# Kernel tuning notes

Measured on AMD Instinct MI355X. Metric: run time of the kernel, lower is better.

The kernel has to match this reference:

```python
import jax, jax.numpy as jnp
import numpy as np
from jax import lax

B, N, D = 4, 4096, 1024
H, DH, K = 8, 128, 256  # heads, dim_head, linformer k
KERNEL = 32
PAD = (15, 16)  # torch padding='same' for even kernel: left=(k-1)//2, right=rest


def setup_inputs() -> dict:
    key = jax.random.key(0)
    ks = jax.random.split(key, 7)
    s = 0.02
    return {
        "x": jax.random.normal(ks[0], (B, N, D), dtype=jnp.float32),
        "Wq": jax.random.normal(ks[1], (D, D), dtype=jnp.float32) * s,
        "Wk": jax.random.normal(ks[2], (D, D), dtype=jnp.float32) * s,
        "Wpk": jax.random.normal(ks[3], (K, N, KERNEL), dtype=jnp.float32) * s,
        "bpk": jax.random.normal(ks[4], (K,), dtype=jnp.float32) * s,
        "Wo": jax.random.normal(ks[5], (D, D), dtype=jnp.float32) * s,
        "bo": jax.random.normal(ks[6], (D,), dtype=jnp.float32) * s,
    }


def reference(x, Wq, Wk, Wpk, bpk, Wo, bo):
    b, n, d = x.shape
    # linear projections (torch Linear: y = x @ W.T)
    q = x @ Wq.T                       # (b, n, h*dh)
    keys = x @ Wk.T                    # (b, n, h*dh)
    # Conv1d over feature length with seq positions as channels: (b, n, d) -> (b, k, d)
    keys = lax.conv_general_dilated(
        keys, Wpk, window_strides=(1,), padding=[PAD],
        dimension_numbers=("NCH", "OIH", "NCH"),
    ) + bpk[None, :, None]             # (b, K, h*dh)
    values = keys                      # share_kv=True
    # split heads
    q = q.reshape(b, n, H, DH).transpose(0, 2, 1, 3)        # (b, h, n, dh)
    kk = keys.reshape(b, K, H, DH).transpose(0, 2, 1, 3)    # (b, h, K, dh)
    vv = values.reshape(b, K, H, DH).transpose(0, 2, 1, 3)  # (b, h, K, dh)
    dots = jnp.einsum("bhnd,bhkd->bhnk", q, kk) * (DH ** -0.5)
    attn = jax.nn.softmax(dots, axis=-1)                    # dropout p=0.0 (eval)
    out = jnp.einsum("bhnk,bhkd->bhnd", attn, vv)
    out = out.transpose(0, 2, 1, 3).reshape(b, n, H * DH)
    return out @ Wo.T + bo
```

## Files before the change

kernel.cpp:

```cpp
#include <hip/hip_runtime.h>


typedef short v8s __attribute__((ext_vector_type(8)));
typedef float v4f __attribute__((ext_vector_type(4)));

#define MFMA16(a, b, c) __builtin_amdgcn_mfma_f32_16x16x32_bf16((a), (b), (c), 0, 0, 0)

__device__ __forceinline__ unsigned short f2bf(float f) {
  unsigned int u = __float_as_uint(f);
  u += 0x7fffu + ((u >> 16) & 1u);
  return (unsigned short)(u >> 16);
}

__device__ __forceinline__ v8s cvt8(float4 a, float4 b) {
  v8s v;
  v[0] = (short)f2bf(a.x); v[1] = (short)f2bf(a.y);
  v[2] = (short)f2bf(a.z); v[3] = (short)f2bf(a.w);
  v[4] = (short)f2bf(b.x); v[5] = (short)f2bf(b.y);
  v[6] = (short)f2bf(b.z); v[7] = (short)f2bf(b.w);
  return v;
}

__global__ __launch_bounds__(256) void k_reorder_wpk(const float* __restrict__ Wpk,
                                                     short* __restrict__ Wr) {
  __shared__ short T[64][40];
  const int k  = blockIdx.x >> 6;
  const int n0 = (blockIdx.x & 63) << 6;
  const int tid = threadIdx.x;
  {
    const int i = tid >> 2, t0 = (tid & 3) << 3;
    const float* p = Wpk + ((size_t)k * 4096 + n0 + i) * 32 + t0;
    float4 a = *(const float4*)p, b = *(const float4*)(p + 4);
    *(v8s*)&T[i][t0] = cvt8(a, b);
  }
  __syncthreads();
  {
    const int t = tid >> 3, j0 = (tid & 7) << 3;
    v8s o;
#pragma unroll
    for (int q = 0; q < 8; ++q) o[q] = T[j0 + q][t];
    *(v8s*)(Wr + ((size_t)t * 256 + k) * 4096 + n0 + j0) = o;
  }
}

__global__ __launch_bounds__(256) void k_init_kc(const float* __restrict__ bpk,
                                                 float* __restrict__ Kc) {
  const int idx = (blockIdx.x * 256 + threadIdx.x) * 4;
  const float v = bpk[(idx >> 10) & 255];
  float4 f; f.x = v; f.y = v; f.z = v; f.w = v;
  *(float4*)(Kc + idx) = f;
}

__global__ __launch_bounds__(256) void k_gemm_qk(const float* __restrict__ x,
                                                 const float* __restrict__ Wq,
                                                 const float* __restrict__ Wk,
                                                 short* __restrict__ Qbf,
                                                 short* __restrict__ Kp) {
  __shared__ short As[128][40];
  __shared__ short Bs[128][40];
  const int tid = threadIdx.x;
  const int m0 = blockIdx.x * 128;
  const int j0 = blockIdx.y * 128;
  const int lane = tid & 63, w = tid >> 6;
  const int wr = (w >> 1) * 64, wc = (w & 1) * 64;
  const int l15 = lane & 15, lg8 = (lane >> 4) * 8;

  v4f acc[4][4];
#pragma unroll
  for (int i = 0; i < 4; ++i)
#pragma unroll
    for (int j = 0; j < 4; ++j) acc[i][j] = (v4f)0.0f;

  for (int k0 = 0; k0 < 1024; k0 += 32) {
#pragma unroll
    for (int c = 0; c < 2; ++c) {
      const int cid = tid + (c << 8);
      const int r = cid >> 2, sg = (cid & 3) << 3;
      const float* pa = x + (size_t)(m0 + r) * 1024 + k0 + sg;
      *(v8s*)&As[r][sg] = cvt8(*(const float4*)pa, *(const float4*)(pa + 4));
      const int J = j0 + r;
      const float* pb = (J < 1024 ? Wq + (size_t)J * 1024
                                  : Wk + (size_t)(J - 1024) * 1024) + k0 + sg;
      *(v8s*)&Bs[r][sg] = cvt8(*(const float4*)pb, *(const float4*)(pb + 4));
    }
    __syncthreads();
    v8s af[4], bfr[4];
#pragma unroll
    for (int mi = 0; mi < 4; ++mi) af[mi] = *(const v8s*)&As[wr + mi * 16 + l15][lg8];
#pragma unroll
    for (int ni = 0; ni < 4; ++ni) bfr[ni] = *(const v8s*)&Bs[wc + ni * 16 + l15][lg8];
#pragma unroll
    for (int ni = 0; ni < 4; ++ni)
#pragma unroll
      for (int mi = 0; mi < 4; ++mi)
        acc[mi][ni] = MFMA16(af[mi], bfr[ni], acc[mi][ni]);
    __syncthreads();
  }
  const int rbase = (lane >> 4) * 4;
#pragma unroll
  for (int mi = 0; mi < 4; ++mi)
#pragma unroll
    for (int ni = 0; ni < 4; ++ni) {
      const int col = j0 + wc + ni * 16 + l15;
      short* dst = (col < 1024) ? Qbf : Kp;
      const int cj = (col < 1024) ? col : col - 1024;
#pragma unroll
      for (int r = 0; r < 4; ++r) {
        const int row = m0 + wr + mi * 16 + rbase + r;
        dst[(size_t)row * 1024 + cj] = (short)f2bf(acc[mi][ni][r]);
      }
    }
}

__global__ __launch_bounds__(256) void k_transpose(const short* __restrict__ src,
                                                   short* __restrict__ dst,
                                                   int R, int C) {
  __shared__ short T[64][72];
  const int r0 = blockIdx.x * 64, c0 = blockIdx.y * 64;
  const size_t sb = (size_t)blockIdx.z * R * C;
  const int tid = threadIdx.x;
  {
    const int i = tid >> 2, q = (tid & 3) << 4;
    const short* ps = src + sb + (size_t)(r0 + i) * C + c0 + q;
    *(v8s*)&T[i][q]     = *(const v8s*)ps;
    *(v8s*)&T[i][q + 8] = *(const v8s*)(ps + 8);
  }
  __syncthreads();
  {
    const int j = tid >> 2, p = (tid & 3) << 4;
    v8s o0, o1;
#pragma unroll
    for (int t = 0; t < 8; ++t) o0[t] = T[p + t][j];
#pragma unroll
    for (int t = 0; t < 8; ++t) o1[t] = T[p + 8 + t][j];
    short* pd = dst + sb + (size_t)(c0 + j) * R + r0 + p;
    *(v8s*)pd = o0;
    *(v8s*)(pd + 8) = o1;
  }
}

__global__ __launch_bounds__(256) void k_conv(const short* __restrict__ Wr,
                                              const short* __restrict__ KpT,
                                              float* __restrict__ Kc) {
  __shared__ short Kt[159][40];
  __shared__ short As[4][128][40];
  const int bx = blockIdx.x;
  const int b = bx & 3, ns = (bx >> 2) & 7, nt = (bx >> 5) & 7, mt = bx >> 8;
  const int K0 = mt * 128, D0 = nt * 128;
  const int tid = threadIdx.x;
  const int lane = tid & 63, w = tid >> 6;
  const int wr = (w >> 1) * 64, wc = (w & 1) * 64;
  const int l15 = lane & 15, lg8 = (lane >> 4) * 8;
  const size_t kpt_b = (size_t)b * 1024 * 4096;

  v4f acc[4][4];
#pragma unroll
  for (int i = 0; i < 4; ++i)
#pragma unroll
    for (int j = 0; j < 4; ++j) acc[i][j] = (v4f)0.0f;

#pragma unroll 1
  for (int nc = 0; nc < 16; ++nc) {
    const int n0 = ns * 512 + nc * 32;
    __syncthreads();
#pragma unroll
    for (int it = 0; it < 3; ++it) {
      const int s = it * 256 + tid;
      if (s < 636) {
        const int r = s >> 2, sg = (s & 3) << 3;
        const int dp = D0 - 15 + r;
        v8s v = {0, 0, 0, 0, 0, 0, 0, 0};
        if (dp >= 0 && dp < 1024)
          v = *(const v8s*)(KpT + kpt_b + (size_t)dp * 4096 + n0 + sg);
        *(v8s*)&Kt[r][sg] = v;
      }
    }
#pragma unroll 1
    for (int tc = 0; tc < 8; ++tc) {
      const int t0 = tc * 4;
      __syncthreads();
#pragma unroll
      for (int i = 0; i < 8; ++i) {
        const int s = i * 256 + tid;
        const int tt = s >> 9, rr = (s >> 2) & 127, sg = (s & 3) << 3;
        *(v8s*)&As[tt][rr][sg] =
            *(const v8s*)(Wr + ((size_t)(t0 + tt) * 256 + K0 + rr) * 4096 + n0 + sg);
      }
      __syncthreads();
#pragma unroll
      for (int tt = 0; tt < 4; ++tt) {
        const int s = t0 + tt;
        v8s af[4], bfr[4];
#pragma unroll
        for (int mi = 0; mi < 4; ++mi)
          af[mi] = *(const v8s*)&As[tt][wr + mi * 16 + l15][lg8];
#pragma unroll
        for (int ni = 0; ni < 4; ++ni)
          bfr[ni] = *(const v8s*)&Kt[wc + ni * 16 + l15 + s][lg8];
#pragma unroll
        for (int ni = 0; ni < 4; ++ni)
#pragma unroll
          for (int mi = 0; mi < 4; ++mi)
            acc[mi][ni] = MFMA16(af[mi], bfr[ni], acc[mi][ni]);
      }
    }
  }
  float* kcb = Kc + (size_t)b * 256 * 1024;
  const int rbase = (lane >> 4) * 4;
#pragma unroll
  for (int mi = 0; mi < 4; ++mi)
#pragma unroll
    for (int ni = 0; ni < 4; ++ni)
#pragma unroll
      for (int r = 0; r < 4; ++r)
        atomicAdd(kcb + (size_t)(K0 + wr + mi * 16 + rbase + r) * 1024 +
                      (D0 + wc + ni * 16 + l15),
                  acc[mi][ni][r]);
}

__global__ __launch_bounds__(256) void k_kc_post(const float* __restrict__ Kc,
                                                 short* __restrict__ Kcbf,
                                                 short* __restrict__ KcT) {
  __shared__ short T[64][72];
  const int k0 = blockIdx.x * 64, d0 = blockIdx.y * 64, b = blockIdx.z;
  const int tid = threadIdx.x;
  {
    const int i = tid >> 2, q = (tid & 3) << 4;
    const float* ps = Kc + (size_t)(b * 256 + k0 + i) * 1024 + d0 + q;
    float4 f0 = *(const float4*)ps,       f1 = *(const float4*)(ps + 4);
    float4 f2 = *(const float4*)(ps + 8), f3 = *(const float4*)(ps + 12);
    v8s v0 = cvt8(f0, f1), v1 = cvt8(f2, f3);
    *(v8s*)&T[i][q] = v0;
    *(v8s*)&T[i][q + 8] = v1;
    short* pc = Kcbf + (size_t)(b * 256 + k0 + i) * 1024 + d0 + q;
    *(v8s*)pc = v0;
    *(v8s*)(pc + 8) = v1;
  }
  __syncthreads();
  {
    const int j = tid >> 2, p = (tid & 3) << 4;
    v8s o0, o1;
#pragma unroll
    for (int t = 0; t < 8; ++t) o0[t] = T[p + t][j];
#pragma unroll
    for (int t = 0; t < 8; ++t) o1[t] = T[p + 8 + t][j];
    short* pd = KcT + (size_t)(b * 1024 + d0 + j) * 256 + k0 + p;
    *(v8s*)pd = o0;
    *(v8s*)(pd + 8) = o1;
  }
}

__global__ __launch_bounds__(256) void k_attn(const short* __restrict__ Qbf,
                                              const short* __restrict__ Kcbf,
                                              const short* __restrict__ KcT,
                                              short* __restrict__ AO) {
  __shared__ short P[4][16][264];
  const int nt = blockIdx.x, h = blockIdx.y, b = blockIdx.z;
  const int tid = threadIdx.x, lane = tid & 63, w = tid >> 6;
  const int l15 = lane & 15, lg4 = (lane >> 4) * 4, lg8 = (lane >> 4) * 8;
  const float scale = 0.08838834764831845f;
  const size_t qb  = (size_t)b * 4096 * 1024 + (size_t)h * 128;
  const size_t kb  = (size_t)b * 256 * 1024 + (size_t)h * 128;
  const size_t vtb = ((size_t)b * 1024 + (size_t)h * 128) * 256;
  short (*Pw)[264] = P[w];
  const int n_wave = nt * 128 + w * 32;

#pragma unroll 1
  for (int half = 0; half < 2; ++half) {
    const int nbase = n_wave + half * 16;
    v8s aq[4];
#pragma unroll
    for (int kt = 0; kt < 4; ++kt)
      aq[kt] = *(const v8s*)(Qbf + qb + (size_t)(nbase + l15) * 1024 + kt * 32 + lg8);

    v4f dacc[16];
#pragma unroll
    for (int ct = 0; ct < 16; ++ct) dacc[ct] = (v4f)0.0f;
#pragma unroll 1
    for (int kt = 0; kt < 4; ++kt) {
#pragma unroll
      for (int ct = 0; ct < 16; ++ct) {
        v8s bk = *(const v8s*)(Kcbf + kb + (size_t)(ct * 16 + l15) * 1024 + kt * 32 + lg8);
        dacc[ct] = MFMA16(aq[kt], bk, dacc[ct]);
      }
    }
#pragma unroll
    for (int ct = 0; ct < 16; ++ct) dacc[ct] = dacc[ct] * scale;
    v4f m4 = dacc[0];
#pragma unroll
    for (int ct = 1; ct < 16; ++ct)
#pragma unroll
      for (int r = 0; r < 4; ++r) m4[r] = fmaxf(m4[r], dacc[ct][r]);
#pragma unroll
    for (int off = 1; off < 16; off <<= 1)
#pragma unroll
      for (int r = 0; r < 4; ++r) m4[r] = fmaxf(m4[r], __shfl_xor(m4[r], off, 64));
    v4f ssum = (v4f)0.0f;
#pragma unroll
    for (int ct = 0; ct < 16; ++ct)
#pragma unroll
      for (int r = 0; r < 4; ++r) {
        const float e = __expf(dacc[ct][r] - m4[r]);
        ssum[r] += e;
        Pw[lg4 + r][ct * 16 + l15] = (short)f2bf(e);
      }
#pragma unroll
    for (int off = 1; off < 16; off <<= 1)
#pragma unroll
      for (int r = 0; r < 4; ++r) ssum[r] += __shfl_xor(ssum[r], off, 64);
    __syncthreads();

    v4f oacc[8];
#pragma unroll
    for (int ct = 0; ct < 8; ++ct) oacc[ct] = (v4f)0.0f;
#pragma unroll 1
    for (int kt2 = 0; kt2 < 8; ++kt2) {
      v8s pa = *(const v8s*)&Pw[l15][kt2 * 32 + lg8];
#pragma unroll
      for (int ct = 0; ct < 8; ++ct) {
        v8s bv = *(const v8s*)(KcT + vtb + (size_t)(ct * 16 + l15) * 256 + kt2 * 32 + lg8);
        oacc[ct] = MFMA16(pa, bv, oacc[ct]);
      }
    }
    v4f inv;
#pragma unroll
    for (int r = 0; r < 4; ++r) inv[r] = 1.0f / ssum[r];
#pragma unroll
    for (int ct = 0; ct < 8; ++ct)
#pragma unroll
      for (int r = 0; r < 4; ++r)
        AO[qb + (size_t)(nbase + lg4 + r) * 1024 + ct * 16 + l15] =
            (short)f2bf(oacc[ct][r] * inv[r]);
    __syncthreads();
  }
}

__global__ __launch_bounds__(256) void k_gemm_out(const short* __restrict__ AO,
                                                  const float* __restrict__ Wo,
                                                  const float* __restrict__ bo,
                                                  float* __restrict__ out) {
  __shared__ short As[128][40];
  __shared__ short Bs[128][40];
  const int tid = threadIdx.x;
  const int m0 = blockIdx.x * 128;
  const int j0 = blockIdx.y * 128;
  const int lane = tid & 63, w = tid >> 6;
  const int wr = (w >> 1) * 64, wc = (w & 1) * 64;
  const int l15 = lane & 15, lg8 = (lane >> 4) * 8;

  v4f acc[4][4];
#pragma unroll
  for (int i = 0; i < 4; ++i)
#pragma unroll
    for (int j = 0; j < 4; ++j) acc[i][j] = (v4f)0.0f;

  for (int k0 = 0; k0 < 1024; k0 += 32) {
#pragma unroll
    for (int c = 0; c < 2; ++c) {
      const int cid = tid + (c << 8);
      const int r = cid >> 2, sg = (cid & 3) << 3;
      *(v8s*)&As[r][sg] = *(const v8s*)(AO + (size_t)(m0 + r) * 1024 + k0 + sg);
      const float* pb = Wo + (size_t)(j0 + r) * 1024 + k0 + sg;
      *(v8s*)&Bs[r][sg] = cvt8(*(const float4*)pb, *(const float4*)(pb + 4));
    }
    __syncthreads();
    v8s af[4], bfr[4];
#pragma unroll
    for (int mi = 0; mi < 4; ++mi) af[mi] = *(const v8s*)&As[wr + mi * 16 + l15][lg8];
#pragma unroll
    for (int ni = 0; ni < 4; ++ni) bfr[ni] = *(const v8s*)&Bs[wc + ni * 16 + l15][lg8];
#pragma unroll
    for (int ni = 0; ni < 4; ++ni)
#pragma unroll
      for (int mi = 0; mi < 4; ++mi)
        acc[mi][ni] = MFMA16(af[mi], bfr[ni], acc[mi][ni]);
    __syncthreads();
  }
  const int rbase = (lane >> 4) * 4;
#pragma unroll
  for (int mi = 0; mi < 4; ++mi)
#pragma unroll
    for (int ni = 0; ni < 4; ++ni) {
      const int col = j0 + wc + ni * 16 + l15;
      const float bias = bo[col];
#pragma unroll
      for (int r = 0; r < 4; ++r) {
        const int row = m0 + wr + mi * 16 + rbase + r;
        out[(size_t)row * 1024 + col] = acc[mi][ni][r] + bias;
      }
    }
}

extern "C" void kernel_launch(void* const* d_in, const int* in_sizes, int n_in,
                              void* d_out, int out_size, void* d_ws, size_t ws_size,
                              hipStream_t stream) {
  const float* x   = (const float*)d_in[0];
  const float* Wq  = (const float*)d_in[1];
  const float* Wk  = (const float*)d_in[2];
  const float* Wpk = (const float*)d_in[3];
  const float* bpk = (const float*)d_in[4];
  const float* Wo  = (const float*)d_in[5];
  const float* bo  = (const float*)d_in[6];

  const size_t OFF_WR   = 0;
  const size_t OFF_QBF  = 67108864;
  const size_t OFF_KP   = 100663296;
  const size_t OFF_KPT  = 134217728;
  const size_t OFF_KC   = 167772160;
  const size_t OFF_KCBF = 171966464;
  const size_t OFF_KCT  = 174063616;
  const size_t NEED     = 176160768;
  if (ws_size < NEED) return;

  char* ws = (char*)d_ws;
  short* Wr   = (short*)(ws + OFF_WR);
  short* Qbf  = (short*)(ws + OFF_QBF);
  short* Kp   = (short*)(ws + OFF_KP);
  short* KpT  = (short*)(ws + OFF_KPT);
  float* Kc   = (float*)(ws + OFF_KC);
  short* Kcbf = (short*)(ws + OFF_KCBF);
  short* KcT  = (short*)(ws + OFF_KCT);
  short* AO   = Kp;
  float* outp = (float*)d_out;

  k_reorder_wpk<<<dim3(16384), dim3(256), 0, stream>>>(Wpk, Wr);
  k_init_kc<<<dim3(1024), dim3(256), 0, stream>>>(bpk, Kc);
  k_gemm_qk<<<dim3(128, 16), dim3(256), 0, stream>>>(x, Wq, Wk, Qbf, Kp);
  k_transpose<<<dim3(64, 16, 4), dim3(256), 0, stream>>>(Kp, KpT, 4096, 1024);
  k_conv<<<dim3(512), dim3(256), 0, stream>>>(Wr, KpT, Kc);
  k_kc_post<<<dim3(4, 16, 4), dim3(256), 0, stream>>>(Kc, Kcbf, KcT);
  k_attn<<<dim3(32, 8, 4), dim3(256), 0, stream>>>(Qbf, Kcbf, KcT, AO);
  k_gemm_out<<<dim3(128, 8), dim3(256), 0, stream>>>(AO, Wo, bo, outp);
}
```

Baseline: 741.0 us.

## Double-buffer GEMMs and conv with direct global-to-LDS loads and swizzled layout

Converts x, Wq/Wk and Wo to bf16 in separate passes so the GEMMs can stream bf16 tiles with global_load_lds into double-buffered, XOR-swizzled LDS. This overlaps loads with MFMA work and avoids bank conflicts. The conv kernel gets the same treatment, plus a zero-padded transposed K buffer that removes boundary checks and an XCD-aware block remapping. It adds extra conversion and padding launches and reuses workspace regions, which carries an aliasing risk.

```diff
diff --git a/kernel.cpp b/kernel.cpp
--- a/kernel.cpp
+++ b/kernel.cpp
@@ -21,6 +21,24 @@
   return v;
 }
 
+__device__ __forceinline__ void gld16(void* lds, const void* g) {
+  __builtin_amdgcn_global_load_lds(
+      (const __attribute__((address_space(1))) void*)g,
+      (__attribute__((address_space(3))) void*)lds, 16, 0, 0);
+}
+
+__device__ __forceinline__ const v8s* frag_ptr(const short* base, int row, int g) {
+  return (const v8s*)(base + row * 32 + (((g ^ (row >> 1)) & 3) << 3));
+}
+
+__global__ __launch_bounds__(256) void k_cvt(const float* __restrict__ src,
+                                             short* __restrict__ dst, int n8) {
+  const int i = blockIdx.x * 256 + threadIdx.x;
+  if (i >= n8) return;
+  const float4* s = (const float4*)src;
+  ((v8s*)dst)[i] = cvt8(s[2 * i], s[2 * i + 1]);
+}
+
 __global__ __launch_bounds__(256) void k_reorder_wpk(const float* __restrict__ Wpk,
                                                      short* __restrict__ Wr) {
   __shared__ short T[64][40];
@@ -51,19 +69,26 @@
   *(float4*)(Kc + idx) = f;
 }
 
-__global__ __launch_bounds__(256) void k_gemm_qk(const float* __restrict__ x,
-                                                 const float* __restrict__ Wq,
-                                                 const float* __restrict__ Wk,
-                                                 short* __restrict__ Qbf,
-                                                 short* __restrict__ Kp) {
-  __shared__ short As[128][40];
-  __shared__ short Bs[128][40];
-  const int tid = threadIdx.x;
-  const int m0 = blockIdx.x * 128;
-  const int j0 = blockIdx.y * 128;
-  const int lane = tid & 63, w = tid >> 6;
+__global__ __launch_bounds__(256) void k_zero_pad(short* __restrict__ KpTp) {
+  const int idx = blockIdx.x * 256 + threadIdx.x;
+  const int ridx = idx >> 9, col8 = idx & 511;
+  const int b = ridx >> 5, rr = ridx & 31;
+  const int row = (rr < 15) ? rr : 1039 + (rr - 15);
+  v8s z = {0, 0, 0, 0, 0, 0, 0, 0};
+  *(v8s*)(KpTp + ((size_t)b * 1056 + row) * 4096 + col8 * 8) = z;
+}
+
+__global__ __launch_bounds__(256) void k_gemm_qk_v2(const short* __restrict__ xbf,
+                                                    const short* __restrict__ Wqk,
+                                                    short* __restrict__ Qbf,
+                                                    short* __restrict__ Kp) {
+  __shared__ short As[2][128][32];
+  __shared__ short Bs[2][128][32];
+  const int tid = threadIdx.x, lane = tid & 63, w = tid >> 6;
+  const int m0 = blockIdx.x * 128, j0 = blockIdx.y * 128;
   const int wr = (w >> 1) * 64, wc = (w & 1) * 64;
-  const int l15 = lane & 15, lg8 = (lane >> 4) * 8;
+  const int l15 = lane & 15, g = lane >> 4;
+  const int sr = lane >> 2, sseg = lane & 3;
 
   v4f acc[4][4];
 #pragma unroll
@@ -71,29 +96,33 @@
 #pragma unroll
     for (int j = 0; j < 4; ++j) acc[i][j] = (v4f)0.0f;
 
-  for (int k0 = 0; k0 < 1024; k0 += 32) {
-#pragma unroll
-    for (int c = 0; c < 2; ++c) {
-      const int cid = tid + (c << 8);
-      const int r = cid >> 2, sg = (cid & 3) << 3;
-      const float* pa = x + (size_t)(m0 + r) * 1024 + k0 + sg;
-      *(v8s*)&As[r][sg] = cvt8(*(const float4*)pa, *(const float4*)(pa + 4));
-      const int J = j0 + r;
-      const float* pb = (J < 1024 ? Wq + (size_t)J * 1024
-                                  : Wk + (size_t)(J - 1024) * 1024) + k0 + sg;
-      *(v8s*)&Bs[r][sg] = cvt8(*(const float4*)pb, *(const float4*)(pb + 4));
-    }
-    __syncthreads();
-    v8s af[4], bfr[4];
-#pragma unroll
-    for (int mi = 0; mi < 4; ++mi) af[mi] = *(const v8s*)&As[wr + mi * 16 + l15][lg8];
-#pragma unroll
-    for (int ni = 0; ni < 4; ++ni) bfr[ni] = *(const v8s*)&Bs[wc + ni * 16 + l15][lg8];
+  auto stage = [&](int buf, int k0) {
+#pragma unroll
+    for (int q0 = 0; q0 < 2; ++q0) {
+      const int rblk = (w * 2 + q0) << 4, r = rblk + sr;
+      const int co = ((sseg ^ (r >> 1)) & 3) << 3;
+      gld16(&As[buf][rblk][0], xbf + (size_t)(m0 + r) * 1024 + k0 + co);
+      gld16(&Bs[buf][rblk][0], Wqk + (size_t)(j0 + r) * 1024 + k0 + co);
+    }
+  };
+
+  stage(0, 0);
+  __syncthreads();
+#pragma unroll 1
+  for (int k0 = 0, buf = 0; k0 < 1024; k0 += 32, buf ^= 1) {
+    if (k0 + 32 < 1024) stage(buf ^ 1, k0 + 32);
+    v8s af[4], bf4[4];
+#pragma unroll
+    for (int mi = 0; mi < 4; ++mi)
+      af[mi] = *frag_ptr(&As[buf][0][0], wr + mi * 16 + l15, g);
 #pragma unroll
     for (int ni = 0; ni < 4; ++ni)
+      bf4[ni] = *frag_ptr(&Bs[buf][0][0], wc + ni * 16 + l15, g);
+#pragma unroll
+    for (int ni = 0; ni < 4; ++ni)
 #pragma unroll
       for (int mi = 0; mi < 4; ++mi)
-        acc[mi][ni] = MFMA16(af[mi], bfr[ni], acc[mi][ni]);
+        acc[mi][ni] = MFMA16(af[mi], bf4[ni], acc[mi][ni]);
     __syncthreads();
   }
   const int rbase = (lane >> 4) * 4;
@@ -112,16 +141,14 @@
     }
 }
 
-__global__ __launch_bounds__(256) void k_transpose(const short* __restrict__ src,
-                                                   short* __restrict__ dst,
-                                                   int R, int C) {
+__global__ __launch_bounds__(256) void k_transpose_pad(const short* __restrict__ src,
+                                                       short* __restrict__ dst) {
   __shared__ short T[64][72];
-  const int r0 = blockIdx.x * 64, c0 = blockIdx.y * 64;
-  const size_t sb = (size_t)blockIdx.z * R * C;
+  const int r0 = blockIdx.x * 64, c0 = blockIdx.y * 64, b = blockIdx.z;
   const int tid = threadIdx.x;
   {
     const int i = tid >> 2, q = (tid & 3) << 4;
-    const short* ps = src + sb + (size_t)(r0 + i) * C + c0 + q;
+    const short* ps = src + ((size_t)b * 4096 + r0 + i) * 1024 + c0 + q;
     *(v8s*)&T[i][q]     = *(const v8s*)ps;
     *(v8s*)&T[i][q + 8] = *(const v8s*)(ps + 8);
   }
@@ -133,25 +160,27 @@
     for (int t = 0; t < 8; ++t) o0[t] = T[p + t][j];
 #pragma unroll
     for (int t = 0; t < 8; ++t) o1[t] = T[p + 8 + t][j];
-    short* pd = dst + sb + (size_t)(c0 + j) * R + r0 + p;
+    short* pd = dst + ((size_t)b * 1056 + 15 + c0 + j) * 4096 + r0 + p;
     *(v8s*)pd = o0;
     *(v8s*)(pd + 8) = o1;
   }
 }
 
-__global__ __launch_bounds__(256) void k_conv(const short* __restrict__ Wr,
-                                              const short* __restrict__ KpT,
-                                              float* __restrict__ Kc) {
-  __shared__ short Kt[159][40];
-  __shared__ short As[4][128][40];
-  const int bx = blockIdx.x;
-  const int b = bx & 3, ns = (bx >> 2) & 7, nt = (bx >> 5) & 7, mt = bx >> 8;
+__global__ __launch_bounds__(256) void k_conv_v2(const short* __restrict__ Wr,
+                                                 const short* __restrict__ KpTp,
+                                                 float* __restrict__ Kc) {
+  __shared__ short As[2][2][128][32];
+  __shared__ short Kt[2][160][32];
+  const int L = blockIdx.x;
+  const int xcd = L & 7, jj = L >> 3;
+  const int slice = xcd + ((jj >> 5) << 3), win = jj & 31;
+  const int mt = slice >> 3, ns = slice & 7, nt = win >> 2, b = win & 3;
   const int K0 = mt * 128, D0 = nt * 128;
-  const int tid = threadIdx.x;
-  const int lane = tid & 63, w = tid >> 6;
+  const int tid = threadIdx.x, lane = tid & 63, w = tid >> 6;
   const int wr = (w >> 1) * 64, wc = (w & 1) * 64;
-  const int l15 = lane & 15, lg8 = (lane >> 4) * 8;
-  const size_t kpt_b = (size_t)b * 1024 * 4096;
+  const int l15 = lane & 15, g = lane >> 4;
+  const int sr = lane >> 2, sseg = lane & 3;
+  const short* KpTb = KpTp + (size_t)b * 1056 * 4096;
 
   v4f acc[4][4];
 #pragma unroll
@@ -159,52 +188,59 @@
 #pragma unroll
     for (int j = 0; j < 4; ++j) acc[i][j] = (v4f)0.0f;
 
-#pragma unroll 1
-  for (int nc = 0; nc < 16; ++nc) {
+  auto stageAs = [&](int buf, int nc, int tp) {
+    const int n0 = ns * 512 + nc * 32, t0 = tp * 2;
+#pragma unroll
+    for (int q0 = 0; q0 < 4; ++q0) {
+      const int q = w + q0 * 4;
+      const int pl = q >> 3, rblk = (q & 7) << 4, r = rblk + sr;
+      gld16(&As[buf][pl][rblk][0],
+            Wr + ((size_t)(t0 + pl) * 256 + K0 + r) * 4096 + n0 +
+                (((sseg ^ (r >> 1)) & 3) << 3));
+    }
+  };
+  auto stageKt = [&](int buf, int nc) {
     const int n0 = ns * 512 + nc * 32;
+    for (int q = w; q < 10; q += 4) {
+      const int rblk = q << 4, r = rblk + sr;
+      gld16(&Kt[buf][rblk][0],
+            KpTb + (size_t)(D0 + r) * 4096 + n0 + (((sseg ^ (r >> 1)) & 3) << 3));
+    }
+  };
+
+  stageKt(0, 0);
+  stageAs(0, 0, 0);
+  __syncthreads();
+  int ab = 0, kb = 0;
+#pragma unroll 1
+  for (int ph = 0; ph < 256; ++ph) {
+    const int tp = ph & 15;
+    if (ph < 255) {
+      const int nn = (ph + 1) >> 4, np = (ph + 1) & 15;
+      stageAs(ab ^ 1, nn, np);
+      if (np == 0) stageKt(kb ^ 1, nn);
+    }
+#pragma unroll
+    for (int pl = 0; pl < 2; ++pl) {
+      const int t = tp * 2 + pl;
+      v8s af[4], bf4[4];
+#pragma unroll
+      for (int mi = 0; mi < 4; ++mi)
+        af[mi] = *frag_ptr(&As[ab][pl][0][0], wr + mi * 16 + l15, g);
+#pragma unroll
+      for (int ni = 0; ni < 4; ++ni)
+        bf4[ni] = *frag_ptr(&Kt[kb][0][0], wc + ni * 16 + l15 + t, g);
+#pragma unroll
+      for (int ni = 0; ni < 4; ++ni)
+#pragma unroll
+        for (int mi = 0; mi < 4; ++mi)
+          acc[mi][ni] = MFMA16(af[mi], bf4[ni], acc[mi][ni]);
+    }
     __syncthreads();
-#pragma unroll
-    for (int it = 0; it < 3; ++it) {
-      const int s = it * 256 + tid;
-      if (s < 636) {
-        const int r = s >> 2, sg = (s & 3) << 3;
-        const int dp = D0 - 15 + r;
-        v8s v = {0, 0, 0, 0, 0, 0, 0, 0};
-        if (dp >= 0 && dp < 1024)
-          v = *(const v8s*)(KpT + kpt_b + (size_t)dp * 4096 + n0 + sg);
-        *(v8s*)&Kt[r][sg] = v;
-      }
-    }
-#pragma unroll 1
-    for (int tc = 0; tc < 8; ++tc) {
-      const int t0 = tc * 4;
-      __syncthreads();
-#pragma unroll
-      for (int i = 0; i < 8; ++i) {
-        const int s = i * 256 + tid;
-        const int tt = s >> 9, rr = (s >> 2) & 127, sg = (s & 3) << 3;
-        *(v8s*)&As[tt][rr][sg] =
-            *(const v8s*)(Wr + ((size_t)(t0 + tt) * 256 + K0 + rr) * 4096 + n0 + sg);
-      }
-      __syncthreads();
-#pragma unroll
-      for (int tt = 0; tt < 4; ++tt) {
-        const int s = t0 + tt;
-        v8s af[4], bfr[4];
-#pragma unroll
-        for (int mi = 0; mi < 4; ++mi)
-          af[mi] = *(const v8s*)&As[tt][wr + mi * 16 + l15][lg8];
-#pragma unroll
-        for (int ni = 0; ni < 4; ++ni)
-          bfr[ni] = *(const v8s*)&Kt[wc + ni * 16 + l15 + s][lg8];
-#pragma unroll
-        for (int ni = 0; ni < 4; ++ni)
-#pragma unroll
-          for (int mi = 0; mi < 4; ++mi)
-            acc[mi][ni] = MFMA16(af[mi], bfr[ni], acc[mi][ni]);
-      }
-    }
-  }
+    ab ^= 1;
+    kb ^= (tp == 15) ? 1 : 0;
+  }
+
   float* kcb = Kc + (size_t)b * 256 * 1024;
   const int rbase = (lane >> 4) * 4;
 #pragma unroll
@@ -335,18 +371,17 @@
   }
 }
 
-__global__ __launch_bounds__(256) void k_gemm_out(const short* __restrict__ AO,
-                                                  const float* __restrict__ Wo,
-                                                  const float* __restrict__ bo,
-                                                  float* __restrict__ out) {
-  __shared__ short As[128][40];
-  __shared__ short Bs[128][40];
-  const int tid = threadIdx.x;
-  const int m0 = blockIdx.x * 128;
-  const int j0 = blockIdx.y * 128;
-  const int lane = tid & 63, w = tid >> 6;
+__global__ __launch_bounds__(256) void k_gemm_out_v2(const short* __restrict__ AO,
+                                                     const short* __restrict__ Wobf,
+                                                     const float* __restrict__ bo,
+                                                     float* __restrict__ out) {
+  __shared__ short As[2][128][32];
+  __shared__ short Bs[2][128][32];
+  const int tid = threadIdx.x, lane = tid & 63, w = tid >> 6;
+  const int m0 = blockIdx.x * 128, j0 = blockIdx.y * 128;
   const int wr = (w >> 1) * 64, wc = (w & 1) * 64;
-  const int l15 = lane & 15, lg8 = (lane >> 4) * 8;
+  const int l15 = lane & 15, g = lane >> 4;
+  const int sr = lane >> 2, sseg = lane & 3;
 
   v4f acc[4][4];
 #pragma unroll
@@ -354,26 +389,33 @@
 #pragma unroll
     for (int j = 0; j < 4; ++j) acc[i][j] = (v4f)0.0f;
 
-  for (int k0 = 0; k0 < 1024; k0 += 32) {
-#pragma unroll
-    for (int c = 0; c < 2; ++c) {
-      const int cid = tid + (c << 8);
-      const int r = cid >> 2, sg = (cid & 3) << 3;
-      *(v8s*)&As[r][sg] = *(const v8s*)(AO + (size_t)(m0 + r) * 1024 + k0 + sg);
-      const float* pb = Wo + (size_t)(j0 + r) * 1024 + k0 + sg;
-      *(v8s*)&Bs[r][sg] = cvt8(*(const float4*)pb, *(const float4*)(pb + 4));
-    }
-    __syncthreads();
-    v8s af[4], bfr[4];
-#pragma unroll
-    for (int mi = 0; mi < 4; ++mi) af[mi] = *(const v8s*)&As[wr + mi * 16 + l15][lg8];
-#pragma unroll
-    for (int ni = 0; ni < 4; ++ni) bfr[ni] = *(const v8s*)&Bs[wc + ni * 16 + l15][lg8];
+  auto stage = [&](int buf, int k0) {
+#pragma unroll
+    for (int q0 = 0; q0 < 2; ++q0) {
+      const int rblk = (w * 2 + q0) << 4, r = rblk + sr;
+      const int co = ((sseg ^ (r >> 1)) & 3) << 3;
+      gld16(&As[buf][rblk][0], AO + (size_t)(m0 + r) * 1024 + k0 + co);
+      gld16(&Bs[buf][rblk][0], Wobf + (size_t)(j0 + r) * 1024 + k0 + co);
+    }
+  };
+
+  stage(0, 0);
+  __syncthreads();
+#pragma unroll 1
+  for (int k0 = 0, buf = 0; k0 < 1024; k0 += 32, buf ^= 1) {
+    if (k0 + 32 < 1024) stage(buf ^ 1, k0 + 32);
+    v8s af[4], bf4[4];
+#pragma unroll
+    for (int mi = 0; mi < 4; ++mi)
+      af[mi] = *frag_ptr(&As[buf][0][0], wr + mi * 16 + l15, g);
 #pragma unroll
     for (int ni = 0; ni < 4; ++ni)
+      bf4[ni] = *frag_ptr(&Bs[buf][0][0], wc + ni * 16 + l15, g);
+#pragma unroll
+    for (int ni = 0; ni < 4; ++ni)
 #pragma unroll
       for (int mi = 0; mi < 4; ++mi)
-        acc[mi][ni] = MFMA16(af[mi], bfr[ni], acc[mi][ni]);
+        acc[mi][ni] = MFMA16(af[mi], bf4[ni], acc[mi][ni]);
     __syncthreads();
   }
   const int rbase = (lane >> 4) * 4;
@@ -403,32 +445,43 @@
   const float* bo  = (const float*)d_in[6];
 
   const size_t OFF_WR   = 0;
-  const size_t OFF_QBF  = 67108864;
-  const size_t OFF_KP   = 100663296;
-  const size_t OFF_KPT  = 134217728;
-  const size_t OFF_KC   = 167772160;
-  const size_t OFF_KCBF = 171966464;
-  const size_t OFF_KCT  = 174063616;
+  const size_t OFF_XBF  = 67108864;
+  const size_t OFF_WQK  = 100663296;
+  const size_t OFF_KPTP = 67108864;
+  const size_t OFF_KCBF = 67108864;
+  const size_t OFF_KCT  = 69206016;
+  const size_t OFF_WOBF = 101711872;
+  const size_t OFF_QBF  = 104857600;
+  const size_t OFF_KP   = 138412032;
+  const size_t OFF_KC   = 171966464;
   const size_t NEED     = 176160768;
   if (ws_size < NEED) return;
 
   char* ws = (char*)d_ws;
   short* Wr   = (short*)(ws + OFF_WR);
+  short* xbf  = (short*)(ws + OFF_XBF);
+  short* Wqk  = (short*)(ws + OFF_WQK);
+  short* KpTp = (short*)(ws + OFF_KPTP);
+  short* Kcbf = (short*)(ws + OFF_KCBF);
+  short* KcT  = (short*)(ws + OFF_KCT);
+  short* Wobf = (short*)(ws + OFF_WOBF);
   short* Qbf  = (short*)(ws + OFF_QBF);
   short* Kp   = (short*)(ws + OFF_KP);
-  short* KpT  = (short*)(ws + OFF_KPT);
   float* Kc   = (float*)(ws + OFF_KC);
-  short* Kcbf = (short*)(ws + OFF_KCBF);
-  short* KcT  = (short*)(ws + OFF_KCT);
   short* AO   = Kp;
   float* outp = (float*)d_out;
 
+  k_cvt<<<dim3(8192), dim3(256), 0, stream>>>(x, xbf, 16777216 / 8);
+  k_cvt<<<dim3(512),  dim3(256), 0, stream>>>(Wq, Wqk, 1048576 / 8);
+  k_cvt<<<dim3(512),  dim3(256), 0, stream>>>(Wk, Wqk + 1048576, 1048576 / 8);
   k_reorder_wpk<<<dim3(16384), dim3(256), 0, stream>>>(Wpk, Wr);
   k_init_kc<<<dim3(1024), dim3(256), 0, stream>>>(bpk, Kc);
-  k_gemm_qk<<<dim3(128, 16), dim3(256), 0, stream>>>(x, Wq, Wk, Qbf, Kp);
-  k_transpose<<<dim3(64, 16, 4), dim3(256), 0, stream>>>(Kp, KpT, 4096, 1024);
-  k_conv<<<dim3(512), dim3(256), 0, stream>>>(Wr, KpT, Kc);
+  k_gemm_qk_v2<<<dim3(128, 16), dim3(256), 0, stream>>>(xbf, Wqk, Qbf, Kp);
+  k_transpose_pad<<<dim3(64, 16, 4), dim3(256), 0, stream>>>(Kp, KpTp);
+  k_cvt<<<dim3(512), dim3(256), 0, stream>>>(Wo, Wobf, 1048576 / 8);
+  k_zero_pad<<<dim3(256), dim3(256), 0, stream>>>(KpTp);
+  k_conv_v2<<<dim3(512), dim3(256), 0, stream>>>(Wr, KpTp, Kc);
   k_kc_post<<<dim3(4, 16, 4), dim3(256), 0, stream>>>(Kc, Kcbf, KcT);
   k_attn<<<dim3(32, 8, 4), dim3(256), 0, stream>>>(Qbf, Kcbf, KcT, AO);
-  k_gemm_out<<<dim3(128, 8), dim3(256), 0, stream>>>(AO, Wo, bo, outp);
-}
+  k_gemm_out_v2<<<dim3(128, 8), dim3(256), 0, stream>>>(AO, Wobf, bo, outp);
+}
```

Result: faster. 643.9 us (-13.1%).
